# Kernel tuning notes

Measured on AMD Instinct MI355X. Metric: run time of the kernel, lower is better.

## Reference

```python
import jax, jax.numpy as jnp
import numpy as np

D = 1024      # in_features
H = 4096      # hidden_dims
E = 8         # expert_nums
K = 2         # top_k
B, S = 4, 2048


def setup_inputs() -> dict:
    key = jax.random.key(0)
    ks = jax.random.split(key, 8)
    def lin(k, fan_in, shape):
        bound = 1.0 / np.sqrt(fan_in)
        return jax.random.uniform(k, shape, jnp.float32, -bound, bound)
    return {
        "x":  jax.random.normal(ks[0], (B, S, D), jnp.float32),
        "Wg": lin(ks[1], D, (D, E)),
        "bg": lin(ks[2], D, (E,)),
        "W1": lin(ks[3], D, (E, D, H)),
        "b1": lin(ks[4], D, (E, H)),
        "W2": lin(ks[5], H, (E, H, D)),
        "b2": lin(ks[6], H, (E, D)),
    }


def reference(x, Wg, bg, W1, b1, W2, b2):
    B_, S_, D_ = x.shape
    xt = x.reshape(-1, D_)                                   # [N, D]
    # Router: softmax gating + top-k
    logits = xt @ Wg + bg                                    # [N, E]
    scores = jax.nn.softmax(logits, axis=-1)
    topk_probs, topk_idx = jax.lax.top_k(scores, K)          # [N, K]
    # Dense per-expert FFN (the source runs every expert on all tokens)
    h = jnp.einsum("nd,edh->enh", xt, W1) + b1[:, None, :]   # [E, N, H]
    h = jax.nn.gelu(h, approximate=False)
    eo = jnp.einsum("enh,ehd->end", h, W2) + b2[:, None, :]  # [E, N, D]
    # Gather selected experts per token and combine with gate weights
    eo = jnp.transpose(eo, (1, 0, 2))                        # [N, E, D]
    sel = jnp.take_along_axis(eo, topk_idx[:, :, None], axis=1)  # [N, K, D]
    out = jnp.einsum("nk,nkd->nd", topk_probs, sel)          # [N, D]
    return out.reshape(B_, S_, D_)
```

## Files before the change

### kernel.cpp

```cpp
#include <hip/hip_runtime.h>
#include <hip/hip_bf16.h>
#include <cstdint>
#include <cstddef>

using bf16 = __hip_bfloat16;
using short8 = __attribute__((ext_vector_type(8))) short;
using floatx4 = __attribute__((ext_vector_type(4))) float;

constexpr int D_IN = 1024;
constexpr int H_DIM = 4096;
constexpr int E_NUM = 8;
constexpr int NTOK = 8192;
constexpr int NPAIR = NTOK * 2;
constexpr int MAXTILES = 144;

constexpr size_t OFF_PTOK  = 1024;
constexpr size_t OFF_PPROB = 263168;
constexpr size_t OFF_SCHED = 525312;
constexpr size_t OFF_XBF   = 1048576;
constexpr size_t OFF_W2T   = OFF_XBF + (size_t)NTOK * D_IN * 2;
constexpr size_t OFF_HBUF  = OFF_W2T + (size_t)E_NUM * D_IN * H_DIM * 2;
constexpr size_t OFF_W1T   = OFF_HBUF + (size_t)NPAIR * H_DIM * 2;

__device__ __forceinline__ void cp16(const bf16* g, bf16* s) {
  __builtin_amdgcn_global_load_lds(
      (const __attribute__((address_space(1))) unsigned int*)g,
      (__attribute__((address_space(3))) unsigned int*)s, 16, 0, 0);
}

__global__ __launch_bounds__(256) void transpose_cvt(
    const float* __restrict__ in, bf16* __restrict__ out, int K, int N) {
  __shared__ float tile[32][33];
  const int e = blockIdx.z;
  const float* ip = in + (size_t)e * K * N + (size_t)(blockIdx.y * 32) * N + blockIdx.x * 32;
  bf16* op = out + (size_t)e * K * N + (size_t)(blockIdx.x * 32) * K + blockIdx.y * 32;
  const int tx = threadIdx.x & 31, ty = threadIdx.x >> 5;
#pragma unroll
  for (int r = 0; r < 4; r++)
    tile[ty + r * 8][tx] = ip[(size_t)(ty + r * 8) * N + tx];
  __syncthreads();
#pragma unroll
  for (int r = 0; r < 4; r++)
    op[(size_t)(ty + r * 8) * K + tx] = __float2bfloat16(tile[tx][ty + r * 8]);
}

__global__ __launch_bounds__(256) void router_kernel(
    const float* __restrict__ x, const float* __restrict__ Wg,
    const float* __restrict__ bg, bf16* __restrict__ Xbf,
    int* __restrict__ counts, int* __restrict__ pairTok, float* __restrict__ pairProb) {
  const int lane = threadIdx.x & 63;
  const int n = blockIdx.x * 4 + (threadIdx.x >> 6);
  const float* xr = x + (size_t)n * D_IN;
  bf16* xbr = Xbf + (size_t)n * D_IN;
  float logit[E_NUM];
#pragma unroll
  for (int e = 0; e < E_NUM; e++) logit[e] = 0.f;
#pragma unroll
  for (int i = 0; i < 16; i++) {
    const int d = i * 64 + lane;
    const float xd = xr[d];
    xbr[d] = __float2bfloat16(xd);
    const float4* wr = (const float4*)(Wg + (size_t)d * E_NUM);
    const float4 w0 = wr[0], w1 = wr[1];
    logit[0] += xd * w0.x; logit[1] += xd * w0.y;
    logit[2] += xd * w0.z; logit[3] += xd * w0.w;
    logit[4] += xd * w1.x; logit[5] += xd * w1.y;
    logit[6] += xd * w1.z; logit[7] += xd * w1.w;
  }
#pragma unroll
  for (int e = 0; e < E_NUM; e++) {
#pragma unroll
    for (int off = 32; off >= 1; off >>= 1)
      logit[e] += __shfl_xor(logit[e], off, 64);
  }
  if (lane == 0) {
    float l[E_NUM], mx = -1e30f;
#pragma unroll
    for (int e = 0; e < E_NUM; e++) { l[e] = logit[e] + bg[e]; mx = fmaxf(mx, l[e]); }
    float ex[E_NUM], s = 0.f;
#pragma unroll
    for (int e = 0; e < E_NUM; e++) { ex[e] = expf(l[e] - mx); s += ex[e]; }
    int i0 = 0;
#pragma unroll
    for (int e = 1; e < E_NUM; e++) if (l[e] > l[i0]) i0 = e;
    int i1 = (i0 == 0) ? 1 : 0;
#pragma unroll
    for (int e = 0; e < E_NUM; e++) if (e != i0 && l[e] > l[i1]) i1 = e;
    const float inv = 1.f / s;
    int pos = atomicAdd(&counts[i0], 1);
    pairTok[i0 * NTOK + pos] = n;
    pairProb[i0 * NTOK + pos] = ex[i0] * inv;
    pos = atomicAdd(&counts[i1], 1);
    pairTok[i1 * NTOK + pos] = n | (1 << 15);
    pairProb[i1 * NTOK + pos] = ex[i1] * inv;
  }
}

__global__ void sched_kernel(const int* __restrict__ counts, int* __restrict__ sched) {
  if (threadIdx.x == 0 && blockIdx.x == 0) {
    int* bases = sched;
    int* nTiles = sched + 8;
    int* tileMap = sched + 16;
    int base = 0, t = 0;
    for (int e = 0; e < E_NUM; e++) {
      bases[e] = base;
      const int nt = (counts[e] + 127) >> 7;
      for (int m = 0; m < nt; m++) tileMap[t++] = (e << 16) | m;
      base += counts[e];
    }
    *nTiles = t;
  }
}

template <int MODE, int K, int NC, int NTX>
__global__ __launch_bounds__(256) void gemm_kernel(
    const bf16* __restrict__ A, const bf16* __restrict__ Wt,
    const float* __restrict__ bias, const int* __restrict__ counts,
    const int* __restrict__ pairTok, const float* __restrict__ pairProb,
    const int* __restrict__ sched, bf16* __restrict__ Hout, float* __restrict__ Out) {
  const int nblk = blockIdx.x % NTX;
  const int tix = blockIdx.x / NTX;
  if (tix >= sched[8]) return;
  const int packed = sched[16 + tix];
  const int e = packed >> 16;
  const int m0 = (packed & 0xFFFF) * 128;
  const int cnt = counts[e];
  const int base = sched[e];
  const int n0 = nblk * 128;

  __shared__ __align__(16) bf16 As[128 * 32];
  __shared__ __align__(16) bf16 Bs[128 * 32];

  const int t = threadIdx.x;
  const int lane = t & 63;
  const int wave = t >> 6;
  const int wmq = wave >> 1, wnq = wave & 1;
  const int fr = lane & 15;
  const int kg = (lane >> 4) * 8;

  const bf16* aSrc[2];
  const bf16* bSrc[2];
#pragma unroll
  for (int i = 0; i < 2; i++) {
    const int lin = i * 256 + t;
    const int r = lin >> 2;
    const int c8 = (lin & 3) * 8;
    int p = m0 + r;
    if (p > cnt - 1) p = cnt - 1;
    if (MODE == 0) {
      const int tok = pairTok[e * NTOK + p] & 0x1FFF;
      aSrc[i] = A + (size_t)tok * K + c8;
    } else {
      aSrc[i] = A + (size_t)(base + p) * K + c8;
    }
    bSrc[i] = Wt + ((size_t)e * NC + n0 + r) * K + c8;
  }

  floatx4 acc[4][4];
#pragma unroll
  for (int ti = 0; ti < 4; ti++)
#pragma unroll
    for (int tj = 0; tj < 4; tj++)
      acc[ti][tj] = {0.f, 0.f, 0.f, 0.f};

  for (int k0 = 0; k0 < K; k0 += 32) {
#pragma unroll
    for (int i = 0; i < 2; i++) {
      cp16(aSrc[i] + k0, &As[(size_t)(i * 256 + t) * 8]);
      cp16(bSrc[i] + k0, &Bs[(size_t)(i * 256 + t) * 8]);
    }
    __syncthreads();
    short8 a[4], b[4];
#pragma unroll
    for (int ti = 0; ti < 4; ti++)
      a[ti] = *(const short8*)&As[(wmq * 64 + ti * 16 + fr) * 32 + kg];
#pragma unroll
    for (int tj = 0; tj < 4; tj++)
      b[tj] = *(const short8*)&Bs[(wnq * 64 + tj * 16 + fr) * 32 + kg];
#pragma unroll
    for (int ti = 0; ti < 4; ti++)
#pragma unroll
      for (int tj = 0; tj < 4; tj++)
        acc[ti][tj] = __builtin_amdgcn_mfma_f32_16x16x32_bf16(a[ti], b[tj], acc[ti][tj], 0, 0, 0);
    __syncthreads();
  }

  float bv[4];
#pragma unroll
  for (int tj = 0; tj < 4; tj++)
    bv[tj] = bias[(size_t)e * NC + n0 + wnq * 64 + tj * 16 + fr];

#pragma unroll
  for (int ti = 0; ti < 4; ti++) {
    const int rb = wmq * 64 + ti * 16 + (lane >> 4) * 4;
#pragma unroll
    for (int i = 0; i < 4; i++) {
      const int p = m0 + rb + i;
      if (p < cnt) {
        if (MODE == 0) {
          bf16* orow = Hout + (size_t)(base + p) * NC + n0 + wnq * 64 + fr;
#pragma unroll
          for (int tj = 0; tj < 4; tj++) {
            const float h = acc[ti][tj][i] + bv[tj];
            const float g = 0.5f * h * (1.f + erff(h * 0.70710678118f));
            orow[tj * 16] = __float2bfloat16(g);
          }
        } else {
          const int pt = pairTok[e * NTOK + p];
          const float pr = pairProb[e * NTOK + p];
          const int tok = pt & 0x1FFF;
          float* orow = Out + (size_t)tok * NC + n0 + wnq * 64 + fr;
#pragma unroll
          for (int tj = 0; tj < 4; tj++)
            atomicAdd(&orow[tj * 16], (acc[ti][tj][i] + bv[tj]) * pr);
        }
      }
    }
  }
}

extern "C" void kernel_launch(void* const* d_in, const int* in_sizes, int n_in,
                              void* d_out, int out_size, void* d_ws, size_t ws_size,
                              hipStream_t stream) {
  const float* x  = (const float*)d_in[0];
  const float* Wg = (const float*)d_in[1];
  const float* bg = (const float*)d_in[2];
  const float* W1 = (const float*)d_in[3];
  const float* b1 = (const float*)d_in[4];
  const float* W2 = (const float*)d_in[5];
  const float* b2 = (const float*)d_in[6];
  float* out = (float*)d_out;
  char* ws = (char*)d_ws;

  int*   counts   = (int*)ws;
  int*   pairTok  = (int*)(ws + OFF_PTOK);
  float* pairProb = (float*)(ws + OFF_PPROB);
  int*   sched    = (int*)(ws + OFF_SCHED);
  bf16*  Xbf      = (bf16*)(ws + OFF_XBF);
  bf16*  W2t      = (bf16*)(ws + OFF_W2T);
  bf16*  Hbuf     = (bf16*)(ws + OFF_HBUF);
  bf16*  W1t      = (bf16*)(ws + OFF_W1T);

  hipMemsetAsync(counts, 0, 64, stream);
  hipMemsetAsync(out, 0, (size_t)out_size * sizeof(float), stream);
  transpose_cvt<<<dim3(H_DIM / 32, D_IN / 32, E_NUM), 256, 0, stream>>>(W1, W1t, D_IN, H_DIM);
  transpose_cvt<<<dim3(D_IN / 32, H_DIM / 32, E_NUM), 256, 0, stream>>>(W2, W2t, H_DIM, D_IN);
  router_kernel<<<NTOK / 4, 256, 0, stream>>>(x, Wg, bg, Xbf, counts, pairTok, pairProb);
  sched_kernel<<<1, 64, 0, stream>>>(counts, sched);
  gemm_kernel<0, D_IN, H_DIM, 32><<<32 * MAXTILES, 256, 0, stream>>>(
      Xbf, W1t, b1, counts, pairTok, pairProb, sched, Hbuf, out);
  gemm_kernel<1, H_DIM, D_IN, 8><<<8 * MAXTILES, 256, 0, stream>>>(
      Hbuf, W2t, b2, counts, pairTok, pairProb, sched, Hbuf, out);
}
```

Baseline: 1.013 ms.

## Replace atomic output accumulation with per-slot result buffer and combine kernel

The second GEMM now writes each token's weighted expert output into a per-(token,slot) fp32 buffer instead of issuing atomicAdds on the output, and a new combine kernel sums the two slots. This also drops the output memset. The weight transpose-convert kernel is widened to 64x64 tiles with float4 loads and 16-byte bf16 stores. The GEMM block index is reordered so tiles vary fastest, changing which blocks share weight columns. The result buffer reuses the W1t workspace region, which assumes W1t is dead after the first GEMM, and the combine adds an extra pass over a 64MB buffer.

Result: no change. 1.013 ms (+0.1%).

```diff
diff --git a/kernel.cpp b/kernel.cpp
--- a/kernel.cpp
+++ b/kernel.cpp
@@ -30,18 +30,28 @@
 
 __global__ __launch_bounds__(256) void transpose_cvt(
     const float* __restrict__ in, bf16* __restrict__ out, int K, int N) {
-  __shared__ float tile[32][33];
+  __shared__ float tile[64][65];
   const int e = blockIdx.z;
-  const float* ip = in + (size_t)e * K * N + (size_t)(blockIdx.y * 32) * N + blockIdx.x * 32;
-  bf16* op = out + (size_t)e * K * N + (size_t)(blockIdx.x * 32) * K + blockIdx.y * 32;
-  const int tx = threadIdx.x & 31, ty = threadIdx.x >> 5;
-#pragma unroll
-  for (int r = 0; r < 4; r++)
-    tile[ty + r * 8][tx] = ip[(size_t)(ty + r * 8) * N + tx];
+  const float* ip = in + (size_t)e * K * N + (size_t)(blockIdx.y * 64) * N + blockIdx.x * 64;
+  bf16* op = out + (size_t)e * K * N + (size_t)(blockIdx.x * 64) * K + blockIdx.y * 64;
+  const int tc = threadIdx.x & 15;
+  const int tr = threadIdx.x >> 4;
+#pragma unroll
+  for (int r = 0; r < 4; r++) {
+    const float4 v = *(const float4*)&ip[(size_t)(tr + r * 16) * N + tc * 4];
+    *(float4*)&tile[tr + r * 16][tc * 4] = v;
+  }
   __syncthreads();
-#pragma unroll
-  for (int r = 0; r < 4; r++)
-    op[(size_t)(ty + r * 8) * K + tx] = __float2bfloat16(tile[tx][ty + r * 8]);
+  const int kg = threadIdx.x & 7;
+  const int nb = threadIdx.x >> 3;
+#pragma unroll
+  for (int r = 0; r < 2; r++) {
+    const int n = nb + r * 32;
+    union { short8 v; bf16 h[8]; } u;
+#pragma unroll
+    for (int j = 0; j < 8; j++) u.h[j] = __float2bfloat16(tile[kg * 8 + j][n]);
+    *(short8*)&op[(size_t)n * K + kg * 8] = u.v;
+  }
 }
 
 __global__ __launch_bounds__(256) void router_kernel(
@@ -117,9 +127,9 @@
     const bf16* __restrict__ A, const bf16* __restrict__ Wt,
     const float* __restrict__ bias, const int* __restrict__ counts,
     const int* __restrict__ pairTok, const float* __restrict__ pairProb,
-    const int* __restrict__ sched, bf16* __restrict__ Hout, float* __restrict__ Out) {
-  const int nblk = blockIdx.x % NTX;
-  const int tix = blockIdx.x / NTX;
+    const int* __restrict__ sched, bf16* __restrict__ Hout, float* __restrict__ Rout) {
+  const int tix = blockIdx.x % MAXTILES;
+  const int nblk = blockIdx.x / MAXTILES;
   if (tix >= sched[8]) return;
   const int packed = sched[16 + tix];
   const int e = packed >> 16;
@@ -208,15 +218,24 @@
         } else {
           const int pt = pairTok[e * NTOK + p];
           const float pr = pairProb[e * NTOK + p];
-          const int tok = pt & 0x1FFF;
-          float* orow = Out + (size_t)tok * NC + n0 + wnq * 64 + fr;
+          const int tok = pt & 0x1FFF, slot = (pt >> 15) & 1;
+          float* orow = Rout + ((size_t)(tok * 2 + slot)) * NC + n0 + wnq * 64 + fr;
 #pragma unroll
           for (int tj = 0; tj < 4; tj++)
-            atomicAdd(&orow[tj * 16], (acc[ti][tj][i] + bv[tj]) * pr);
+            orow[tj * 16] = (acc[ti][tj][i] + bv[tj]) * pr;
         }
       }
     }
   }
+}
+
+__global__ __launch_bounds__(256) void combine_kernel(
+    const float4* __restrict__ r, float4* __restrict__ o) {
+  const int j = blockIdx.x * 256 + threadIdx.x;
+  const int n = j >> 8, c = j & 255;
+  const float4 a = r[(size_t)(n * 2) * 256 + c];
+  const float4 b = r[(size_t)(n * 2 + 1) * 256 + c];
+  o[j] = make_float4(a.x + b.x, a.y + b.y, a.z + b.z, a.w + b.w);
 }
 
 extern "C" void kernel_launch(void* const* d_in, const int* in_sizes, int n_in,
@@ -240,15 +259,16 @@
   bf16*  W2t      = (bf16*)(ws + OFF_W2T);
   bf16*  Hbuf     = (bf16*)(ws + OFF_HBUF);
   bf16*  W1t      = (bf16*)(ws + OFF_W1T);
+  float* resbuf   = (float*)W1t;
 
   hipMemsetAsync(counts, 0, 64, stream);
-  hipMemsetAsync(out, 0, (size_t)out_size * sizeof(float), stream);
-  transpose_cvt<<<dim3(H_DIM / 32, D_IN / 32, E_NUM), 256, 0, stream>>>(W1, W1t, D_IN, H_DIM);
-  transpose_cvt<<<dim3(D_IN / 32, H_DIM / 32, E_NUM), 256, 0, stream>>>(W2, W2t, H_DIM, D_IN);
+  transpose_cvt<<<dim3(H_DIM / 64, D_IN / 64, E_NUM), 256, 0, stream>>>(W1, W1t, D_IN, H_DIM);
+  transpose_cvt<<<dim3(D_IN / 64, H_DIM / 64, E_NUM), 256, 0, stream>>>(W2, W2t, H_DIM, D_IN);
   router_kernel<<<NTOK / 4, 256, 0, stream>>>(x, Wg, bg, Xbf, counts, pairTok, pairProb);
   sched_kernel<<<1, 64, 0, stream>>>(counts, sched);
   gemm_kernel<0, D_IN, H_DIM, 32><<<32 * MAXTILES, 256, 0, stream>>>(
-      Xbf, W1t, b1, counts, pairTok, pairProb, sched, Hbuf, out);
+      Xbf, W1t, b1, counts, pairTok, pairProb, sched, Hbuf, resbuf);
   gemm_kernel<1, H_DIM, D_IN, 8><<<8 * MAXTILES, 256, 0, stream>>>(
-      Hbuf, W2t, b2, counts, pairTok, pairProb, sched, Hbuf, out);
-}
+      Hbuf, W2t, b2, counts, pairTok, pairProb, sched, Hbuf, resbuf);
+  combine_kernel<<<(NTOK * D_IN / 4) / 256, 256, 0, stream>>>((const float4*)resbuf, (float4*)out);
+}
```
